# Kernel optimization log

Hardware: AMD Instinct MI355X
Metric: run time of the kernel (lower is better)

## Reference

```python
import jax, jax.numpy as jnp
import numpy as np

N, E, H, G, C = 50000, 800000, 512, 64, 2
BERT = 768


def setup_inputs() -> dict:
    key = jax.random.key(0)
    ks = jax.random.split(key, 12)
    sem = jax.random.normal(ks[0], (N, BERT), jnp.float32)
    mask = jax.random.randint(ks[1], (N, 1), 0, 2).astype(jnp.float32)
    x = jnp.concatenate([sem, mask], axis=1)  # [N, 769]
    edge_index = jax.random.randint(ks[2], (2, E), 0, N)
    batch = jnp.sort(jax.random.randint(ks[3], (N,), 0, G))
    s = lambda k, shp, fan: jax.random.normal(k, shp, jnp.float32) / np.float32(np.sqrt(fan))
    return dict(
        x=x, edge_index=edge_index, batch=batch,
        sem_W=s(ks[4], (BERT, H), BERT), sem_b=jnp.zeros((H,), jnp.float32),
        slice_emb=jax.random.normal(ks[5], (2, H), jnp.float32),
        ln_g=jnp.ones((H,), jnp.float32), ln_b=jnp.zeros((H,), jnp.float32),
        conv1_W=s(ks[6], (H, H), H), conv1_b=jnp.zeros((H,), jnp.float32),
        conv2_W=s(ks[7], (H, H), H), conv2_b=jnp.zeros((H,), jnp.float32),
        cls_W1=s(ks[8], (H, H), H), cls_b1=jnp.zeros((H,), jnp.float32),
        cls_W2=s(ks[9], (H, C), H), cls_b2=jnp.zeros((C,), jnp.float32),
    )


def _layer_norm(x, g, b, eps=1e-5):
    m = x.mean(-1, keepdims=True)
    v = x.var(-1, keepdims=True)
    return (x - m) * jax.lax.rsqrt(v + eps) * g + b


def _gcn_conv(h, src, dst, W, b):
    # PyG GCNConv: add self-loops, sym-normalized aggregation of X @ W, plus bias
    hw = h @ W  # [N, H]
    deg = jnp.zeros((N,), hw.dtype).at[dst].add(1.0) + 1.0  # +1 self-loop
    dinv = jax.lax.rsqrt(deg)
    coef = dinv[src] * dinv[dst]  # [E]
    agg = jax.ops.segment_sum(hw[src] * coef[:, None], dst, num_segments=N)
    agg = agg + hw * (dinv * dinv)[:, None]  # self-loop contribution
    return agg + b


def reference(x, edge_index, batch, sem_W, sem_b, slice_emb, ln_g, ln_b,
              conv1_W, conv1_b, conv2_W, conv2_b, cls_W1, cls_b1, cls_W2, cls_b2):
    sem = x[:, :BERT]
    idx = x[:, BERT].astype(jnp.int32)  # binary slice mask
    h = sem @ sem_W + sem_b + slice_emb[idx]
    h = jax.nn.gelu(_layer_norm(h, ln_g, ln_b), approximate=False)
    src, dst = edge_index[0], edge_index[1]
    h = jax.nn.gelu(_gcn_conv(h, src, dst, conv1_W, conv1_b), approximate=False)
    h2 = jax.nn.gelu(_gcn_conv(h, src, dst, conv2_W, conv2_b), approximate=False)
    h = h + h2  # residual (args.residual=True)
    sums = jax.ops.segment_sum(h, batch, num_segments=G)
    cnt = jax.ops.segment_sum(jnp.ones((N,), h.dtype), batch, num_segments=G)
    hg = sums / jnp.maximum(cnt, 1.0)[:, None]  # global mean pool [G, H]
    z = jax.nn.gelu(hg @ cls_W1 + cls_b1, approximate=False)
    return z @ cls_W2 + cls_b2  # [G, C]
```

## Files before the change

kernel.cpp:

```cpp
#include <hip/hip_runtime.h>
#include <hip/hip_bf16.h>

typedef unsigned short u16;
typedef __bf16 bfv8 __attribute__((ext_vector_type(8)));
typedef float f32x4 __attribute__((ext_vector_type(4)));
typedef unsigned int u32x4 __attribute__((ext_vector_type(4)));

#define HH 512
#define BERT_D 768
#define XSTRIDE 769

__device__ __forceinline__ float gelu_f(float x) {
  return 0.5f * x * (1.0f + erff(x * 0.70710678118654752440f));
}
__device__ __forceinline__ float us2f(u16 u) {
  union { unsigned int i; float f; } c; c.i = ((unsigned int)u) << 16; return c.f;
}
__device__ __forceinline__ u16 f2us(float f) {
  union { float f; unsigned int i; } c; c.f = f;
  unsigned int i = c.i;
  i += 0x7FFFu + ((i >> 16) & 1u);
  return (u16)(i >> 16);
}
__device__ __forceinline__ void gl_lds16(const u16* g, u16* l) {
  __builtin_amdgcn_global_load_lds((const __attribute__((address_space(1))) void*)g,
                                   (__attribute__((address_space(3))) void*)l, 16, 0, 0);
}

__global__ void k_idx(const float* __restrict__ x, int* __restrict__ idx, int Nn) {
  int i = blockIdx.x * blockDim.x + threadIdx.x;
  if (i < Nn) idx[i] = (int)x[(size_t)i * XSTRIDE + BERT_D];
}

__global__ void k_transpose_bf16(const float* __restrict__ src, u16* __restrict__ dst,
                                 int K, int Nn) {
  int i = blockIdx.x * blockDim.x + threadIdx.x;
  if (i >= K * Nn) return;
  int k = i / Nn, j = i - k * Nn;
  dst[(size_t)j * K + k] = f2us(src[i]);
}

__global__ void k_deg(const int* __restrict__ dst, int* __restrict__ deg, int E) {
  int e = blockIdx.x * blockDim.x + threadIdx.x;
  if (e < E) atomicAdd(&deg[dst[e]], 1);
}

__launch_bounds__(256)
__global__ void k_part(const int* __restrict__ deg, int* __restrict__ part, int Nn) {
  const int i = blockIdx.x * 256 + threadIdx.x;
  int v = (i < Nn) ? deg[i] : 0;
#pragma unroll
  for (int o = 32; o; o >>= 1) v += __shfl_xor(v, o);
  __shared__ int ws4[4];
  if ((threadIdx.x & 63) == 0) ws4[threadIdx.x >> 6] = v;
  __syncthreads();
  if (threadIdx.x == 0) part[blockIdx.x] = ws4[0] + ws4[1] + ws4[2] + ws4[3];
}

__launch_bounds__(256)
__global__ void k_scan_part(int* __restrict__ part, int* __restrict__ row_ptr,
                            int nb, int Nn) {
  __shared__ int sm[256];
  const int t = threadIdx.x;
  int v = (t < nb) ? part[t] : 0;
  sm[t] = v;
  __syncthreads();
  for (int d = 1; d < 256; d <<= 1) {
    int u = (t >= d) ? sm[t - d] : 0;
    __syncthreads();
    sm[t] += u;
    __syncthreads();
  }
  if (t < nb) part[t] = sm[t] - v;
  if (t == 255) row_ptr[Nn] = sm[255];
}

__launch_bounds__(256)
__global__ void k_scan_write(const int* __restrict__ deg, const int* __restrict__ part,
                             int* __restrict__ row_ptr, int* __restrict__ cursor,
                             float* __restrict__ dinv, int Nn) {
  __shared__ int sm[256];
  const int t = threadIdx.x;
  const int i = blockIdx.x * 256 + t;
  int v = (i < Nn) ? deg[i] : 0;
  sm[t] = v;
  __syncthreads();
  for (int d = 1; d < 256; d <<= 1) {
    int u = (t >= d) ? sm[t - d] : 0;
    __syncthreads();
    sm[t] += u;
    __syncthreads();
  }
  if (i < Nn) {
    int pre = part[blockIdx.x] + sm[t] - v;
    row_ptr[i] = pre;
    cursor[i] = pre;
    dinv[i] = rsqrtf((float)v + 1.0f);
  }
}

__global__ void k_csr(const int* __restrict__ src, const int* __restrict__ dst,
                      int* __restrict__ cursor, int* __restrict__ csr_src, int E) {
  int e = blockIdx.x * blockDim.x + threadIdx.x;
  if (e >= E) return;
  int d = dst[e];
  int pos = atomicAdd(&cursor[d], 1);
  csr_src[pos] = src[e];
}


__launch_bounds__(256, 2)
__global__ void k_gemm1(const float* __restrict__ xf,
                        const u16* __restrict__ B, int ldb,
                        u16* __restrict__ C, int M,
                        const float* __restrict__ bias,
                        const float* __restrict__ emb,
                        const int* __restrict__ idx) {
  __shared__ alignas(16) u16 As[128 * 64];
  __shared__ alignas(16) u16 Bs[256 * 64];
  const int t = threadIdx.x;
  const int l = t & 63;
  const int w = t >> 6;
  const int wro = (w >> 1) * 64;
  const int wco = (w & 1) * 128;
  const int lr = l & 15;
  const int kq = l >> 4;
  const int rsw = lr & 7;
  const int nwg = gridDim.x;
  const int id = blockIdx.x;
  const int q8 = nwg >> 3, r8 = nwg & 7;
  const int xcd = id & 7, rk = id >> 3;
  const int swz = (xcd < r8 ? xcd * (q8 + 1) : r8 * (q8 + 1) + (xcd - r8) * q8) + rk;
  const int brow = (swz >> 1) * 128;
  const int bcol = (swz & 1) * 256;

  const int bsw8 = (((t & 7) ^ ((t >> 3) & 7)) * 8);
  const int arr = t >> 4;
  const int ac4 = (t & 15) * 4;
  const int asub = (t & 1) * 4;
  const int aswz = (((t & 15) >> 1) ^ (arr & 7)) * 8;

  f32x4 acc[4][8] = {};

  for (int k0 = 0; k0 < BERT_D; k0 += 64) {
#pragma unroll
    for (int i = 0; i < 8; ++i) {
      const int eo = (i * 256 + t) * 8;
      const int r = eo >> 6;
      gl_lds16(B + (size_t)(bcol + r) * ldb + (k0 + bsw8), Bs + eo);
    }
#pragma unroll
    for (int i = 0; i < 8; ++i) {
      const int rr = i * 16 + arr;
      int gr = brow + rr;
      if (gr > M - 1) gr = M - 1;
      const float* xp = xf + (size_t)gr * XSTRIDE + k0 + ac4;
      float f0 = xp[0], f1 = xp[1], f2 = xp[2], f3 = xp[3];
      union { u16 h[4]; unsigned long long q; } pk;
      pk.h[0] = f2us(f0); pk.h[1] = f2us(f1); pk.h[2] = f2us(f2); pk.h[3] = f2us(f3);
      *(unsigned long long*)(As + rr * 64 + aswz + asub) = pk.q;
    }
    __syncthreads();
#pragma unroll
    for (int ks = 0; ks < 2; ++ks) {
      bfv8 af[4], bfr[8];
      const int rg = ((ks * 4 + kq) ^ rsw) * 8;
#pragma unroll
      for (int m = 0; m < 4; ++m)
        af[m] = __builtin_bit_cast(bfv8, *(const uint4*)(As + (wro + m * 16 + lr) * 64 + rg));
#pragma unroll
      for (int n = 0; n < 8; ++n)
        bfr[n] = __builtin_bit_cast(bfv8, *(const uint4*)(Bs + (wco + n * 16 + lr) * 64 + rg));
#pragma unroll
      for (int m = 0; m < 4; ++m)
#pragma unroll
        for (int n = 0; n < 8; ++n)
          acc[m][n] = __builtin_amdgcn_mfma_f32_16x16x32_bf16(af[m], bfr[n], acc[m][n], 0, 0, 0);
    }
    __syncthreads();
  }

#pragma unroll
  for (int m = 0; m < 4; ++m) {
#pragma unroll
    for (int r = 0; r < 4; ++r) {
      const int row = brow + wro + m * 16 + (l >> 4) * 4 + r;
      if (row >= M) continue;
#pragma unroll
      for (int n = 0; n < 8; ++n) {
        const int col = bcol + wco + n * 16 + lr;
        float v = acc[m][n][r] + bias[col] + emb[idx[row] * HH + col];
        C[(size_t)row * HH + col] = f2us(v);
      }
    }
  }
}

template <int EPI>
__launch_bounds__(256, 2)
__global__ void k_gemm_bt(const u16* __restrict__ A, int lda,
                          const u16* __restrict__ B, int ldb,
                          u16* __restrict__ C, int M, int Kd,
                          const float* __restrict__ dscale) {
  __shared__ alignas(16) u16 As[128 * 64];
  __shared__ alignas(16) u16 Bs[256 * 64];
  const int t = threadIdx.x;
  const int l = t & 63;
  const int w = t >> 6;
  const int wro = (w >> 1) * 64;
  const int wco = (w & 1) * 128;
  const int lr = l & 15;
  const int kq = l >> 4;
  const int rsw = lr & 7;
  const int nwg = gridDim.x;
  const int id = blockIdx.x;
  const int q8 = nwg >> 3, r8 = nwg & 7;
  const int xcd = id & 7, rk = id >> 3;
  const int swz = (xcd < r8 ? xcd * (q8 + 1) : r8 * (q8 + 1) + (xcd - r8) * q8) + rk;
  const int brow = (swz >> 1) * 128;
  const int bcol = (swz & 1) * 256;

  const int ssw8 = (((t & 7) ^ ((t >> 3) & 7)) * 8);

  f32x4 acc[4][8] = {};

  for (int k0 = 0; k0 < Kd; k0 += 64) {
#pragma unroll
    for (int i = 0; i < 4; ++i) {
      const int eo = (i * 256 + t) * 8;
      const int r = eo >> 6;
      int gr = brow + r;
      if (gr > M - 1) gr = M - 1;
      gl_lds16(A + (size_t)gr * lda + (k0 + ssw8), As + eo);
    }
#pragma unroll
    for (int i = 0; i < 8; ++i) {
      const int eo = (i * 256 + t) * 8;
      const int r = eo >> 6;
      gl_lds16(B + (size_t)(bcol + r) * ldb + (k0 + ssw8), Bs + eo);
    }
    __syncthreads();
#pragma unroll
    for (int ks = 0; ks < 2; ++ks) {
      bfv8 af[4], bfr[8];
      const int rg = ((ks * 4 + kq) ^ rsw) * 8;
#pragma unroll
      for (int m = 0; m < 4; ++m)
        af[m] = __builtin_bit_cast(bfv8, *(const uint4*)(As + (wro + m * 16 + lr) * 64 + rg));
#pragma unroll
      for (int n = 0; n < 8; ++n)
        bfr[n] = __builtin_bit_cast(bfv8, *(const uint4*)(Bs + (wco + n * 16 + lr) * 64 + rg));
#pragma unroll
      for (int m = 0; m < 4; ++m)
#pragma unroll
        for (int n = 0; n < 8; ++n)
          acc[m][n] = __builtin_amdgcn_mfma_f32_16x16x32_bf16(af[m], bfr[n], acc[m][n], 0, 0, 0);
    }
    __syncthreads();
  }

#pragma unroll
  for (int m = 0; m < 4; ++m) {
#pragma unroll
    for (int r = 0; r < 4; ++r) {
      const int row = brow + wro + m * 16 + (l >> 4) * 4 + r;
      if (row >= M) continue;
      const float sc = (EPI == 2) ? dscale[row] : 1.0f;
#pragma unroll
      for (int n = 0; n < 8; ++n) {
        const int col = bcol + wco + n * 16 + lr;
        float v = acc[m][n][r];
        if (EPI == 2) v *= sc;
        C[(size_t)row * HH + col] = f2us(v);
      }
    }
  }
}

__launch_bounds__(256)
__global__ void k_ln_gelu(const u16* __restrict__ h0, const float* __restrict__ gw,
                          const float* __restrict__ bw, u16* __restrict__ hout, int Nn) {
  const int wid = (int)((blockIdx.x * (long long)blockDim.x + threadIdx.x) >> 6);
  if (wid >= Nn) return;
  const int l = threadIdx.x & 63;
  uint4 q = *(const uint4*)(h0 + (size_t)wid * HH + l * 8);
  const u16* us = (const u16*)&q;
  float f[8]; float s = 0.f, s2 = 0.f;
#pragma unroll
  for (int j = 0; j < 8; ++j) { f[j] = us2f(us[j]); s += f[j]; s2 += f[j] * f[j]; }
#pragma unroll
  for (int o = 32; o; o >>= 1) { s += __shfl_xor(s, o); s2 += __shfl_xor(s2, o); }
  const float mean = s * (1.f / 512.f);
  const float var = s2 * (1.f / 512.f) - mean * mean;
  const float rs = rsqrtf(var + 1e-5f);
  union { u16 ov[8]; uint4 q; } o;
#pragma unroll
  for (int j = 0; j < 8; ++j) {
    int col = l * 8 + j;
    float y = (f[j] - mean) * rs * gw[col] + bw[col];
    o.ov[j] = f2us(gelu_f(y));
  }
  *(uint4*)(hout + (size_t)wid * HH + l * 8) = o.q;
}

__launch_bounds__(256)
__global__ void k_agg(const u16* __restrict__ hwS, const int* __restrict__ row_ptr,
                      const int* __restrict__ csr_src, const float* __restrict__ dinv,
                      const float* __restrict__ bias, u16* __restrict__ hout, int Nn) {
  const int wid = (int)((blockIdx.x * (long long)blockDim.x + threadIdx.x) >> 6);
  if (wid >= Nn) return;
  const int l = threadIdx.x & 63;
  const int cb = l * 8;
  float acc[8] = {0.f, 0.f, 0.f, 0.f, 0.f, 0.f, 0.f, 0.f};
  const int lo = row_ptr[wid], hi = row_ptr[wid + 1];
  const float dv = dinv[wid];
  int e = lo;
  for (; e + 4 <= hi; e += 4) {
    const int u0 = csr_src[e + 0];
    const int u1 = csr_src[e + 1];
    const int u2 = csr_src[e + 2];
    const int u3 = csr_src[e + 3];
    uint4 q0 = *(const uint4*)(hwS + (size_t)u0 * HH + cb);
    uint4 q1 = *(const uint4*)(hwS + (size_t)u1 * HH + cb);
    uint4 q2 = *(const uint4*)(hwS + (size_t)u2 * HH + cb);
    uint4 q3 = *(const uint4*)(hwS + (size_t)u3 * HH + cb);
    const u16* p0 = (const u16*)&q0;
    const u16* p1 = (const u16*)&q1;
    const u16* p2 = (const u16*)&q2;
    const u16* p3 = (const u16*)&q3;
#pragma unroll
    for (int j = 0; j < 8; ++j)
      acc[j] += (us2f(p0[j]) + us2f(p1[j])) + (us2f(p2[j]) + us2f(p3[j]));
  }
  for (; e < hi; ++e) {
    const int u = csr_src[e];
    uint4 q = *(const uint4*)(hwS + (size_t)u * HH + cb);
    const u16* p = (const u16*)&q;
#pragma unroll
    for (int j = 0; j < 8; ++j) acc[j] += us2f(p[j]);
  }
  {
    uint4 q = *(const uint4*)(hwS + (size_t)wid * HH + cb);
    const u16* p = (const u16*)&q;
#pragma unroll
    for (int j = 0; j < 8; ++j) acc[j] += us2f(p[j]);
  }
  union { u16 ov[8]; u32x4 q; } o;
#pragma unroll
  for (int j = 0; j < 8; ++j) {
    float v = acc[j] * dv + bias[cb + j];
    o.ov[j] = f2us(gelu_f(v));
  }
  __builtin_nontemporal_store(o.q, (u32x4*)(hout + (size_t)wid * HH + cb));
}

#define POOL_RS 16
__launch_bounds__(256)
__global__ void k_pool2(const u16* __restrict__ h1, const u16* __restrict__ h2,
                        const int* __restrict__ batch, float* __restrict__ hg, int Nn) {
  const int g = blockIdx.x;
  const int chunk = blockIdx.y;
  const int t = threadIdx.x;
  const int w = t >> 6;
  const int l = t & 63;
  const int cb = l * 8;
  int lo, hi;
  { int a = 0, b = Nn; while (a < b) { int m = (a + b) >> 1; if (batch[m] < g) a = m + 1; else b = m; } lo = a; }
  { int a = 0, b = Nn; while (a < b) { int m = (a + b) >> 1; if (batch[m] < g + 1) a = m + 1; else b = m; } hi = a; }
  const int len = hi - lo;
  const int per = (len + POOL_RS - 1) / POOL_RS;
  const int rlo = lo + chunk * per;
  const int rhi = min(rlo + per, hi);
  float acc[8] = {};
  for (int r = rlo + w; r < rhi; r += 4) {
    u32x4 a = __builtin_nontemporal_load((const u32x4*)(h1 + (size_t)r * HH + cb));
    u32x4 b = __builtin_nontemporal_load((const u32x4*)(h2 + (size_t)r * HH + cb));
    const u16* ua = (const u16*)&a;
    const u16* ub = (const u16*)&b;
#pragma unroll
    for (int j = 0; j < 8; ++j) acc[j] += us2f(ua[j]) + us2f(ub[j]);
  }
  __shared__ float red[4][HH];
#pragma unroll
  for (int j = 0; j < 8; ++j) red[w][cb + j] = acc[j];
  __syncthreads();
  if (w == 0) {
#pragma unroll
    for (int j = 0; j < 8; ++j) {
      const int col = cb + j;
      float s = red[0][col] + red[1][col] + red[2][col] + red[3][col];
      if (s != 0.f) atomicAdd(&hg[(size_t)g * HH + col], s);
    }
  }
}

__launch_bounds__(256)
__global__ void k_cls(const float* __restrict__ hg, const int* __restrict__ batch,
                      const float* __restrict__ W1, const float* __restrict__ b1,
                      const float* __restrict__ W2, const float* __restrict__ b2,
                      float* __restrict__ out, int Nn) {
  const int g = blockIdx.x;
  const int t = threadIdx.x;
  __shared__ float hl[512];
  __shared__ float zl[512];
  __shared__ float pr[512];
  int lo, hi;
  { int a = 0, b = Nn; while (a < b) { int m = (a + b) >> 1; if (batch[m] < g) a = m + 1; else b = m; } lo = a; }
  { int a = 0, b = Nn; while (a < b) { int m = (a + b) >> 1; if (batch[m] < g + 1) a = m + 1; else b = m; } hi = a; }
  const float inv = 1.0f / fmaxf((float)(hi - lo), 1.0f);
  hl[t] = hg[(size_t)g * HH + t] * inv;
  hl[t + 256] = hg[(size_t)g * HH + t + 256] * inv;
  __syncthreads();
#pragma unroll
  for (int jj = 0; jj < 2; ++jj) {
    const int j = t + jj * 256;
    float a = b1[j];
    for (int k = 0; k < 512; ++k) a += hl[k] * W1[k * HH + j];
    zl[j] = gelu_f(a);
  }
  __syncthreads();
  float p0 = 0.f, p1 = 0.f;
  for (int k = t; k < 512; k += 256) { p0 += zl[k] * W2[k * 2]; p1 += zl[k] * W2[k * 2 + 1]; }
  pr[t] = p0; pr[t + 256] = p1;
  __syncthreads();
  for (int s2 = 128; s2; s2 >>= 1) {
    if (t < s2) { pr[t] += pr[t + s2]; pr[t + 256] += pr[t + 256 + s2]; }
    __syncthreads();
  }
  if (t == 0) { out[g * 2] = pr[0] + b2[0]; out[g * 2 + 1] = pr[256] + b2[1]; }
}

extern "C" void kernel_launch(void* const* d_in, const int* in_sizes, int n_in,
                              void* d_out, int out_size, void* d_ws, size_t ws_size,
                              hipStream_t stream) {
  const float* x        = (const float*)d_in[0];
  const int*   eidx     = (const int*)d_in[1];
  const int*   batch    = (const int*)d_in[2];
  const float* sem_W    = (const float*)d_in[3];
  const float* sem_b    = (const float*)d_in[4];
  const float* sl_emb   = (const float*)d_in[5];
  const float* ln_g     = (const float*)d_in[6];
  const float* ln_b     = (const float*)d_in[7];
  const float* W1       = (const float*)d_in[8];
  const float* b1       = (const float*)d_in[9];
  const float* W2       = (const float*)d_in[10];
  const float* b2       = (const float*)d_in[11];
  const float* cW1      = (const float*)d_in[12];
  const float* cb1      = (const float*)d_in[13];
  const float* cW2      = (const float*)d_in[14];
  const float* cb2      = (const float*)d_in[15];
  const int N_ = in_sizes[2];
  const int E_ = in_sizes[1] / 2;
  const int G_ = out_size / 2;
  const int* src = eidx;
  const int* dst = eidx + E_;

  char* ws = (char*)d_ws;
  size_t off = 0;
  auto alloc = [&](size_t bytes) -> void* {
    void* p = (void*)(ws + off);
    off += (bytes + 255) & ~(size_t)255;
    return p;
  };
  u16* h1 = (u16*)alloc((size_t)N_ * HH * sizeof(u16));
  u16* h0 = (u16*)alloc((size_t)N_ * HH * sizeof(u16));
  u16* hw = h0;
  u16* h = (u16*)alloc((size_t)N_ * HH * sizeof(u16));
  u16* h2 = h;
  u16* semW_T = (u16*)alloc((size_t)HH * BERT_D * sizeof(u16));
  u16* W1T    = (u16*)alloc((size_t)HH * HH * sizeof(u16));
  u16* W2T    = (u16*)alloc((size_t)HH * HH * sizeof(u16));
  int* idx     = (int*)alloc((size_t)N_ * 4);
  int* deg     = (int*)alloc((size_t)N_ * 4);
  float* dinv  = (float*)alloc((size_t)N_ * 4);
  int* row_ptr = (int*)alloc((size_t)(N_ + 1) * 4);
  int* cursor  = (int*)alloc((size_t)N_ * 4);
  int* csr_src = (int*)alloc((size_t)E_ * 4);
  int* part    = (int*)alloc(1024);
  float* hg    = (float*)alloc((size_t)G_ * HH * 4);

  hipMemsetAsync(deg, 0, (size_t)N_ * 4, stream);
  hipMemsetAsync(hg, 0, (size_t)G_ * HH * 4, stream);

  k_idx<<<(N_ + 255) / 256, 256, 0, stream>>>(x, idx, N_);
  k_transpose_bf16<<<(BERT_D * HH + 255) / 256, 256, 0, stream>>>(sem_W, semW_T, BERT_D, HH);
  k_transpose_bf16<<<(HH * HH + 255) / 256, 256, 0, stream>>>(W1, W1T, HH, HH);
  k_transpose_bf16<<<(HH * HH + 255) / 256, 256, 0, stream>>>(W2, W2T, HH, HH);

  const int nb = (N_ + 255) / 256;
  k_deg<<<(E_ + 255) / 256, 256, 0, stream>>>(dst, deg, E_);
  k_part<<<nb, 256, 0, stream>>>(deg, part, N_);
  k_scan_part<<<1, 256, 0, stream>>>(part, row_ptr, nb, N_);
  k_scan_write<<<nb, 256, 0, stream>>>(deg, part, row_ptr, cursor, dinv, N_);
  k_csr<<<(E_ + 255) / 256, 256, 0, stream>>>(src, dst, cursor, csr_src, E_);

  const int Mtiles = (N_ + 127) / 128;
  const int wave_blocks = (N_ + 3) / 4;
  const int gemm_grid = Mtiles * 2;

  k_gemm1<<<gemm_grid, 256, 0, stream>>>(
      x, semW_T, BERT_D, h0, N_, sem_b, sl_emb, idx);
  k_ln_gelu<<<wave_blocks, 256, 0, stream>>>(h0, ln_g, ln_b, h, N_);
  k_gemm_bt<2><<<gemm_grid, 256, 0, stream>>>(
      h, HH, W1T, HH, hw, N_, HH, dinv);
  k_agg<<<wave_blocks, 256, 0, stream>>>(hw, row_ptr, csr_src, dinv, b1, h1, N_);
  k_gemm_bt<2><<<gemm_grid, 256, 0, stream>>>(
      h1, HH, W2T, HH, hw, N_, HH, dinv);
  k_agg<<<wave_blocks, 256, 0, stream>>>(hw, row_ptr, csr_src, dinv, b2, h2, N_);
  k_pool2<<<dim3(G_, POOL_RS), 256, 0, stream>>>(h1, h2, batch, hg, N_);
  k_cls<<<G_, 256, 0, stream>>>(hg, batch, cW1, cb1, cW2, cb2, (float*)d_out, N_);
}
```

Baseline: 701.2 us.

## Double-buffer GEMM LDS tiles and use 8-wave blocks with smaller per-wave tiles

The three MFMA GEMMs now use double-buffered LDS tiles, so the next K-slice is loaded while the current one is computed, with one barrier per step instead of two. Blocks grow from 4 to 8 waves, and each wave computes a 64x64 sub-tile instead of 64x128. In the first GEMM the fp32 input is register-prefetched with wider 8-element loads and converted to bf16 after the MFMAs. This roughly doubles LDS use per block (96 KB) and may limit occupancy. The global_load_lds prefetch into the alternate buffer relies on the end-of-iteration barrier for correctness.

```diff
diff --git a/kernel.cpp b/kernel.cpp
--- a/kernel.cpp
+++ b/kernel.cpp
@@ -9,6 +9,9 @@
 #define HH 512
 #define BERT_D 768
 #define XSTRIDE 769
+#define BM 128
+#define BN 256
+#define BK 64
 
 __device__ __forceinline__ float gelu_f(float x) {
   return 0.5f * x * (1.0f + erff(x * 0.70710678118654752440f));
@@ -109,20 +112,20 @@
 }
 
 
-__launch_bounds__(256, 2)
+__launch_bounds__(512, 2)
 __global__ void k_gemm1(const float* __restrict__ xf,
                         const u16* __restrict__ B, int ldb,
                         u16* __restrict__ C, int M,
                         const float* __restrict__ bias,
                         const float* __restrict__ emb,
                         const int* __restrict__ idx) {
-  __shared__ alignas(16) u16 As[128 * 64];
-  __shared__ alignas(16) u16 Bs[256 * 64];
+  __shared__ alignas(16) u16 As[2][BM * BK];
+  __shared__ alignas(16) u16 Bs[2][BN * BK];
   const int t = threadIdx.x;
   const int l = t & 63;
   const int w = t >> 6;
-  const int wro = (w >> 1) * 64;
-  const int wco = (w & 1) * 128;
+  const int wro = (w >> 2) * 64;
+  const int wco = (w & 3) * 64;
   const int lr = l & 15;
   const int kq = l >> 4;
   const int rsw = lr & 7;
@@ -131,53 +134,77 @@
   const int q8 = nwg >> 3, r8 = nwg & 7;
   const int xcd = id & 7, rk = id >> 3;
   const int swz = (xcd < r8 ? xcd * (q8 + 1) : r8 * (q8 + 1) + (xcd - r8) * q8) + rk;
-  const int brow = (swz >> 1) * 128;
-  const int bcol = (swz & 1) * 256;
-
-  const int bsw8 = (((t & 7) ^ ((t >> 3) & 7)) * 8);
-  const int arr = t >> 4;
-  const int ac4 = (t & 15) * 4;
-  const int asub = (t & 1) * 4;
-  const int aswz = (((t & 15) >> 1) ^ (arr & 7)) * 8;
-
-  f32x4 acc[4][8] = {};
-
-  for (int k0 = 0; k0 < BERT_D; k0 += 64) {
-#pragma unroll
-    for (int i = 0; i < 8; ++i) {
-      const int eo = (i * 256 + t) * 8;
-      const int r = eo >> 6;
-      gl_lds16(B + (size_t)(bcol + r) * ldb + (k0 + bsw8), Bs + eo);
-    }
-#pragma unroll
-    for (int i = 0; i < 8; ++i) {
-      const int rr = i * 16 + arr;
-      int gr = brow + rr;
-      if (gr > M - 1) gr = M - 1;
-      const float* xp = xf + (size_t)gr * XSTRIDE + k0 + ac4;
-      float f0 = xp[0], f1 = xp[1], f2 = xp[2], f3 = xp[3];
-      union { u16 h[4]; unsigned long long q; } pk;
-      pk.h[0] = f2us(f0); pk.h[1] = f2us(f1); pk.h[2] = f2us(f2); pk.h[3] = f2us(f3);
-      *(unsigned long long*)(As + rr * 64 + aswz + asub) = pk.q;
-    }
-    __syncthreads();
+  const int brow = (swz >> 1) * BM;
+  const int bcol = (swz & 1) * BN;
+
+  const int ssw8 = (((t & 7) ^ ((t >> 3) & 7)) * 8);
+  const int arow = t >> 2;
+  const int ag0 = (t & 3) * 2;
+  const int arsw = arow & 7;
+
+  int agr = brow + arow; if (agr > M - 1) agr = M - 1;
+  const float* xrow = xf + (size_t)agr * XSTRIDE;
+
+  float av[16];
+
+  f32x4 acc[4][4] = {};
+
+  auto stageB = [&](int k0, int buf) {
+#pragma unroll
+    for (int i = 0; i < 4; ++i) {
+      const int r = i * 64 + (t >> 3);
+      gl_lds16(B + (size_t)(bcol + r) * ldb + (k0 + ssw8), &Bs[buf][(i * 512 + t) * 8]);
+    }
+  };
+  auto loadA = [&](int k0) {
+#pragma unroll
+    for (int j = 0; j < 2; ++j) {
+      const int sg = (ag0 + j) ^ arsw;
+      const float* xp = xrow + k0 + sg * 8;
+#pragma unroll
+      for (int e = 0; e < 8; ++e) av[j * 8 + e] = xp[e];
+    }
+  };
+  auto writeA = [&](int buf) {
+#pragma unroll
+    for (int j = 0; j < 2; ++j) {
+      union { u16 h[8]; uint4 q; } pk;
+#pragma unroll
+      for (int e = 0; e < 8; ++e) pk.h[e] = f2us(av[j * 8 + e]);
+      *(uint4*)(&As[buf][arow * 64 + (ag0 + j) * 8]) = pk.q;
+    }
+  };
+
+  loadA(0);
+  stageB(0, 0);
+  writeA(0);
+  __syncthreads();
+
+  int cur = 0;
+  for (int st = 0; st < BERT_D / BK; ++st) {
+    const bool hn = (st + 1 < BERT_D / BK);
+    if (hn) { loadA((st + 1) * BK); stageB((st + 1) * BK, cur ^ 1); }
+    const u16* Ac = As[cur];
+    const u16* Bc = Bs[cur];
 #pragma unroll
     for (int ks = 0; ks < 2; ++ks) {
-      bfv8 af[4], bfr[8];
+      bfv8 af[4], bfr[4];
       const int rg = ((ks * 4 + kq) ^ rsw) * 8;
 #pragma unroll
       for (int m = 0; m < 4; ++m)
-        af[m] = __builtin_bit_cast(bfv8, *(const uint4*)(As + (wro + m * 16 + lr) * 64 + rg));
-#pragma unroll
-      for (int n = 0; n < 8; ++n)
-        bfr[n] = __builtin_bit_cast(bfv8, *(const uint4*)(Bs + (wco + n * 16 + lr) * 64 + rg));
+        af[m] = __builtin_bit_cast(bfv8, *(const uint4*)(Ac + (wro + m * 16 + lr) * 64 + rg));
+#pragma unroll
+      for (int n = 0; n < 4; ++n)
+        bfr[n] = __builtin_bit_cast(bfv8, *(const uint4*)(Bc + (wco + n * 16 + lr) * 64 + rg));
 #pragma unroll
       for (int m = 0; m < 4; ++m)
 #pragma unroll
-        for (int n = 0; n < 8; ++n)
+        for (int n = 0; n < 4; ++n)
           acc[m][n] = __builtin_amdgcn_mfma_f32_16x16x32_bf16(af[m], bfr[n], acc[m][n], 0, 0, 0);
     }
-    __syncthreads();
+    if (hn) writeA(cur ^ 1);
+    __syncthreads();
+    cur ^= 1;
   }
 
 #pragma unroll
@@ -187,7 +214,7 @@
       const int row = brow + wro + m * 16 + (l >> 4) * 4 + r;
       if (row >= M) continue;
 #pragma unroll
-      for (int n = 0; n < 8; ++n) {
+      for (int n = 0; n < 4; ++n) {
         const int col = bcol + wco + n * 16 + lr;
         float v = acc[m][n][r] + bias[col] + emb[idx[row] * HH + col];
         C[(size_t)row * HH + col] = f2us(v);
@@ -197,18 +224,18 @@
 }
 
 template <int EPI>
-__launch_bounds__(256, 2)
+__launch_bounds__(512, 2)
 __global__ void k_gemm_bt(const u16* __restrict__ A, int lda,
                           const u16* __restrict__ B, int ldb,
                           u16* __restrict__ C, int M, int Kd,
                           const float* __restrict__ dscale) {
-  __shared__ alignas(16) u16 As[128 * 64];
-  __shared__ alignas(16) u16 Bs[256 * 64];
+  __shared__ alignas(16) u16 As[2][BM * BK];
+  __shared__ alignas(16) u16 Bs[2][BN * BK];
   const int t = threadIdx.x;
   const int l = t & 63;
   const int w = t >> 6;
-  const int wro = (w >> 1) * 64;
-  const int wco = (w & 1) * 128;
+  const int wro = (w >> 2) * 64;
+  const int wco = (w & 3) * 64;
   const int lr = l & 15;
   const int kq = l >> 4;
   const int rsw = lr & 7;
@@ -217,46 +244,55 @@
   const int q8 = nwg >> 3, r8 = nwg & 7;
   const int xcd = id & 7, rk = id >> 3;
   const int swz = (xcd < r8 ? xcd * (q8 + 1) : r8 * (q8 + 1) + (xcd - r8) * q8) + rk;
-  const int brow = (swz >> 1) * 128;
-  const int bcol = (swz & 1) * 256;
+  const int brow = (swz >> 1) * BM;
+  const int bcol = (swz & 1) * BN;
 
   const int ssw8 = (((t & 7) ^ ((t >> 3) & 7)) * 8);
-
-  f32x4 acc[4][8] = {};
-
-  for (int k0 = 0; k0 < Kd; k0 += 64) {
+  const int srow = t >> 3;
+
+  f32x4 acc[4][4] = {};
+
+  auto stage = [&](int k0, int buf) {
+#pragma unroll
+    for (int i = 0; i < 2; ++i) {
+      const int r = i * 64 + srow;
+      int gr = brow + r; if (gr > M - 1) gr = M - 1;
+      gl_lds16(A + (size_t)gr * lda + (k0 + ssw8), &As[buf][(i * 512 + t) * 8]);
+    }
 #pragma unroll
     for (int i = 0; i < 4; ++i) {
-      const int eo = (i * 256 + t) * 8;
-      const int r = eo >> 6;
-      int gr = brow + r;
-      if (gr > M - 1) gr = M - 1;
-      gl_lds16(A + (size_t)gr * lda + (k0 + ssw8), As + eo);
-    }
-#pragma unroll
-    for (int i = 0; i < 8; ++i) {
-      const int eo = (i * 256 + t) * 8;
-      const int r = eo >> 6;
-      gl_lds16(B + (size_t)(bcol + r) * ldb + (k0 + ssw8), Bs + eo);
-    }
-    __syncthreads();
+      const int r = i * 64 + srow;
+      gl_lds16(B + (size_t)(bcol + r) * ldb + (k0 + ssw8), &Bs[buf][(i * 512 + t) * 8]);
+    }
+  };
+
+  stage(0, 0);
+  __syncthreads();
+
+  const int nst = Kd / BK;
+  int cur = 0;
+  for (int st = 0; st < nst; ++st) {
+    if (st + 1 < nst) stage((st + 1) * BK, cur ^ 1);
+    const u16* Ac = As[cur];
+    const u16* Bc = Bs[cur];
 #pragma unroll
     for (int ks = 0; ks < 2; ++ks) {
-      bfv8 af[4], bfr[8];
+      bfv8 af[4], bfr[4];
       const int rg = ((ks * 4 + kq) ^ rsw) * 8;
 #pragma unroll
       for (int m = 0; m < 4; ++m)
-        af[m] = __builtin_bit_cast(bfv8, *(const uint4*)(As + (wro + m * 16 + lr) * 64 + rg));
-#pragma unroll
-      for (int n = 0; n < 8; ++n)
-        bfr[n] = __builtin_bit_cast(bfv8, *(const uint4*)(Bs + (wco + n * 16 + lr) * 64 + rg));
+        af[m] = __builtin_bit_cast(bfv8, *(const uint4*)(Ac + (wro + m * 16 + lr) * 64 + rg));
+#pragma unroll
+      for (int n = 0; n < 4; ++n)
+        bfr[n] = __builtin_bit_cast(bfv8, *(const uint4*)(Bc + (wco + n * 16 + lr) * 64 + rg));
 #pragma unroll
       for (int m = 0; m < 4; ++m)
 #pragma unroll
-        for (int n = 0; n < 8; ++n)
+        for (int n = 0; n < 4; ++n)
           acc[m][n] = __builtin_amdgcn_mfma_f32_16x16x32_bf16(af[m], bfr[n], acc[m][n], 0, 0, 0);
     }
     __syncthreads();
+    cur ^= 1;
   }
 
 #pragma unroll
@@ -267,7 +303,7 @@
       if (row >= M) continue;
       const float sc = (EPI == 2) ? dscale[row] : 1.0f;
 #pragma unroll
-      for (int n = 0; n < 8; ++n) {
+      for (int n = 0; n < 4; ++n) {
         const int col = bcol + wco + n * 16 + lr;
         float v = acc[m][n][r];
         if (EPI == 2) v *= sc;
@@ -494,17 +530,17 @@
   k_scan_write<<<nb, 256, 0, stream>>>(deg, part, row_ptr, cursor, dinv, N_);
   k_csr<<<(E_ + 255) / 256, 256, 0, stream>>>(src, dst, cursor, csr_src, E_);
 
-  const int Mtiles = (N_ + 127) / 128;
+  const int Mtiles = (N_ + BM - 1) / BM;
   const int wave_blocks = (N_ + 3) / 4;
-  const int gemm_grid = Mtiles * 2;
-
-  k_gemm1<<<gemm_grid, 256, 0, stream>>>(
+  const int gemm_grid = Mtiles * (HH / BN);
+
+  k_gemm1<<<gemm_grid, 512, 0, stream>>>(
       x, semW_T, BERT_D, h0, N_, sem_b, sl_emb, idx);
   k_ln_gelu<<<wave_blocks, 256, 0, stream>>>(h0, ln_g, ln_b, h, N_);
-  k_gemm_bt<2><<<gemm_grid, 256, 0, stream>>>(
+  k_gemm_bt<2><<<gemm_grid, 512, 0, stream>>>(
       h, HH, W1T, HH, hw, N_, HH, dinv);
   k_agg<<<wave_blocks, 256, 0, stream>>>(hw, row_ptr, csr_src, dinv, b1, h1, N_);
-  k_gemm_bt<2><<<gemm_grid, 256, 0, stream>>>(
+  k_gemm_bt<2><<<gemm_grid, 512, 0, stream>>>(
       h1, HH, W2T, HH, hw, N_, HH, dinv);
   k_agg<<<wave_blocks, 256, 0, stream>>>(hw, row_ptr, csr_src, dinv, b2, h2, N_);
   k_pool2<<<dim3(G_, POOL_RS), 256, 0, stream>>>(h1, h2, batch, hg, N_);
```

New measurement: 782.0 us. 11.5% more time.
